# Kernel optimization log

Hardware: AMD Instinct MI355X
Metric: run time of the kernel (lower is better)

The kernel has to match this reference:

```python
import jax, jax.numpy as jnp
import numpy as np

CHUNK = 2048  # row tile size; keeps the [CHUNK, M] tile ~268 MB


def setup_inputs() -> dict:
    key = jax.random.key(0)
    k1, k2, k3 = jax.random.split(key, 3)
    N, M, D = 32768, 32768, 32
    ls = jax.random.uniform(k1, (1,), dtype=jnp.float32, minval=0.1, maxval=1.0)
    x = jax.random.normal(k2, (N, D), dtype=jnp.float32)
    y = jax.random.normal(k3, (M, D), dtype=jnp.float32)
    return {"ls": ls, "x": x, "y": y}


def reference(ls, x, y):
    # out[i] = sum_j exp(-ls * ||x_i - y_j||^2), computed in row tiles
    # (never materializes the full N x M matrix, like KeOps Genred).
    N, D = x.shape
    y_sq = jnp.sum(y * y, axis=1)  # [M]

    def row_chunk(xc):
        # xc: [CHUNK, D]
        x_sq = jnp.sum(xc * xc, axis=1)  # [CHUNK]
        sq = x_sq[:, None] + y_sq[None, :] - 2.0 * (xc @ y.T)  # [CHUNK, M]
        return jnp.sum(jnp.exp(-ls[0] * sq), axis=1)  # [CHUNK]

    x_tiles = x.reshape(N // CHUNK, CHUNK, D)
    out = jax.lax.map(row_chunk, x_tiles)  # [N//CHUNK, CHUNK]
    return out.reshape(N, 1)
```

## Files before the change

### kernel.cpp

```cpp
#include <hip/hip_runtime.h>
#include <math.h>

#define DIM 32
#define BLK 256
#define JSPLIT 16
#define ITPB 8
#define RI   2
#define GTT  16

typedef _Float16 half8 __attribute__((ext_vector_type(8)));
typedef float    f32x4 __attribute__((ext_vector_type(4)));
typedef float    f32x2 __attribute__((ext_vector_type(2)));

struct hl16 { half8 h; half8 l; };


__global__ __launch_bounds__(BLK) void rbf_prep(
    const float* __restrict__ lsp, const float* __restrict__ x,
    const float* __restrict__ y, int n, int m,
    double* __restrict__ acc, double* __restrict__ scale,
    float* __restrict__ bf, hl16* __restrict__ xhl, hl16* __restrict__ yhl)
{
    int i = blockIdx.x * BLK + threadIdx.x;
    const double c2 = -(double)lsp[0] * 1.4426950408889634074;
    const float mf = (float)(-2.0 * c2);
    if (i < n) {
        const float* xp = x + (size_t)i * DIM;
        double xs = 0.0;
        #pragma unroll
        for (int d = 0; d < DIM; ++d) { double v = (double)xp[d]; xs = fma(v, v, xs); }
        acc[i] = 0.0;
        scale[i] = exp2(c2 * xs);
        const int it = i >> 4, r15 = i & 15;
        #pragma unroll
        for (int q = 0; q < 4; ++q) {
            half8 hh, hl;
            #pragma unroll
            for (int d = 0; d < 8; ++d) {
                float v = xp[q * 8 + d] * mf;
                _Float16 h = (_Float16)v;
                hh[d] = h;
                hl[d] = (_Float16)((v - (float)h) * 4096.0f);
            }
            xhl[it * 64 + q * 16 + r15].h = hh;
            xhl[it * 64 + q * 16 + r15].l = hl;
        }
    }
    if (i < m) {
        const float* yp = y + (size_t)i * DIM;
        double ys = 0.0;
        #pragma unroll
        for (int d = 0; d < DIM; ++d) { double v = (double)yp[d]; ys = fma(v, v, ys); }
        bf[i] = (float)(c2 * ys);
        const int it = i >> 4, r15 = i & 15;
        #pragma unroll
        for (int q = 0; q < 4; ++q) {
            half8 hh, hl;
            #pragma unroll
            for (int d = 0; d < 8; ++d) {
                float v = yp[q * 8 + d];
                _Float16 h = (_Float16)v;
                hh[d] = h;
                hl[d] = (_Float16)((v - (float)h) * 4096.0f);
            }
            yhl[it * 64 + q * 16 + r15].h = hh;
            yhl[it * 64 + q * 16 + r15].l = hl;
        }
    }
}

__global__ __launch_bounds__(BLK, 4) void rbf_main(
    const hl16* __restrict__ xhl, const hl16* __restrict__ yhl,
    const float* __restrict__ bf, double* __restrict__ acc, int chunk_j)
{
    const int lane = threadIdx.x & 63;
    const int wave = threadIdx.x >> 6;
    const int itbase = blockIdx.x * ITPB + wave * RI;
    const int c15 = lane & 15;

    half8 ah[RI], al[RI];
    #pragma unroll
    for (int r = 0; r < RI; ++r) {
        ah[r] = xhl[(itbase + r) * 64 + lane].h;
        al[r] = xhl[(itbase + r) * 64 + lane].l;
    }

    const int jt0 = (blockIdx.y * chunk_j) >> 4;
    const int njt = chunk_j >> 4;

    const f32x4 zq = {0.0f, 0.0f, 0.0f, 0.0f};
    const float k12 = 0x1p-12f;

    double accd[RI][4];
    #pragma unroll
    for (int r = 0; r < RI; ++r)
        #pragma unroll
        for (int e = 0; e < 4; ++e) accd[r][e] = 0.0;

    half8 bh = yhl[(size_t)jt0 * 64 + lane].h;
    half8 bl = yhl[(size_t)jt0 * 64 + lane].l;
    float bfv = bf[jt0 * 16 + c15];

    for (int g = 0; g < njt / GTT; ++g) {
        f32x2 accf[RI][2];
        #pragma unroll
        for (int r = 0; r < RI; ++r) {
            accf[r][0] = (f32x2){0.0f, 0.0f};
            accf[r][1] = (f32x2){0.0f, 0.0f};
        }

        #pragma unroll
        for (int tt = 0; tt < GTT; ++tt) {
            const int jt = jt0 + g * GTT + tt;
            int jn = jt + 1; if (jn >= jt0 + njt) jn = jt0;
            const hl16* __restrict__ yt = yhl + (size_t)jn * 64;
            half8 bh_n = yt[lane].h;
            half8 bl_n = yt[lane].l;
            float bf_n = (bf + jn * 16)[c15];

            const f32x4 cbf = {bfv, bfv, bfv, bfv};
            #pragma unroll
            for (int r = 0; r < RI; ++r) {
                f32x4 cm = __builtin_amdgcn_mfma_f32_16x16x32_f16(ah[r], bh, cbf, 0, 0, 0);
                f32x4 cl = __builtin_amdgcn_mfma_f32_16x16x32_f16(ah[r], bl, zq, 0, 0, 0);
                cl = __builtin_amdgcn_mfma_f32_16x16x32_f16(al[r], bh, cl, 0, 0, 0);
                f32x2 f0 = {cm[0], cm[1]}, f1 = {cm[2], cm[3]};
                f32x2 l0 = {cl[0], cl[1]}, l1 = {cl[2], cl[3]};
                f0 = l0 * k12 + f0;
                f1 = l1 * k12 + f1;
                f32x2 e0 = {__builtin_amdgcn_exp2f(f0.x), __builtin_amdgcn_exp2f(f0.y)};
                f32x2 e1 = {__builtin_amdgcn_exp2f(f1.x), __builtin_amdgcn_exp2f(f1.y)};
                accf[r][0] += e0;
                accf[r][1] += e1;
            }
            bh = bh_n; bl = bl_n; bfv = bf_n;
        }
        #pragma unroll
        for (int r = 0; r < RI; ++r) {
            accd[r][0] += (double)accf[r][0].x;
            accd[r][1] += (double)accf[r][0].y;
            accd[r][2] += (double)accf[r][1].x;
            accd[r][3] += (double)accf[r][1].y;
        }
    }

    #pragma unroll
    for (int r = 0; r < RI; ++r) {
        #pragma unroll
        for (int e = 0; e < 4; ++e) {
            double v = accd[r][e];
            v += __shfl_xor(v, 1, 64);
            v += __shfl_xor(v, 2, 64);
            v += __shfl_xor(v, 4, 64);
            v += __shfl_xor(v, 8, 64);
            if (c15 == 0) {
                int row = (itbase + r) * 16 + (lane >> 4) * 4 + e;
                atomicAdd(&acc[row], v);
            }
        }
    }
}

__global__ __launch_bounds__(BLK) void rbf_finish(
    const double* __restrict__ acc, const double* __restrict__ scale,
    float* __restrict__ out, int n)
{
    int i = blockIdx.x * BLK + threadIdx.x;
    if (i < n) out[i] = (float)(acc[i] * scale[i]);
}

extern "C" void kernel_launch(void* const* d_in, const int* in_sizes, int n_in,
                              void* d_out, int out_size, void* d_ws, size_t ws_size,
                              hipStream_t stream)
{
    const float* ls = (const float*)d_in[0];
    const float* x  = (const float*)d_in[1];
    const float* y  = (const float*)d_in[2];
    const int n = in_sizes[1] / DIM;
    const int m = in_sizes[2] / DIM;
    float* out = (float*)d_out;

    char* ws = (char*)d_ws;
    double* acc   = (double*)ws;
    double* scale = acc + n;
    float*  bf    = (float*)(scale + n);
    hl16*   xhl   = (hl16*)(bf + m);
    hl16*   yhl   = xhl + (size_t)(n / 16) * 64;

    const int nm = (n > m) ? n : m;
    rbf_prep<<<(nm + BLK - 1) / BLK, BLK, 0, stream>>>(
        ls, x, y, n, m, acc, scale, bf, xhl, yhl);

    const int chunk = m / JSPLIT;
    dim3 grid(n / (16 * ITPB), JSPLIT);
    rbf_main<<<grid, BLK, 0, stream>>>(xhl, yhl, bf, acc, chunk);

    rbf_finish<<<(n + BLK - 1) / BLK, BLK, 0, stream>>>(acc, scale, out, n);
}
```

Before: 322.3 us.

## Fuse finish into main kernel, deepen y-tile prefetch, fold bias into low MFMA

Removes the separate finish kernel. Each row-block group now counts completed j-splits with an atomic counter, and the last block scales and writes the outputs itself. The y-tile loads move to a 4-slot ring buffer that prefetches two tiles ahead instead of one. The pre-scaled bias now seeds the low-part MFMA accumulator instead of the main one, and the occupancy hint drops from 4 to 3 blocks per CU. In exchange the code adds fences and atomics at block end and more live registers, and the prefetch reads two tiles past each chunk, which is why the workspace is reordered so y data comes before x data.

```diff
diff --git a/kernel.cpp b/kernel.cpp
--- a/kernel.cpp
+++ b/kernel.cpp
@@ -4,8 +4,8 @@
 #define DIM 32
 #define BLK 256
 #define JSPLIT 16
-#define ITPB 8
 #define RI   2
+#define ITPB (4*RI)
 #define GTT  16
 
 typedef _Float16 half8 __attribute__((ext_vector_type(8)));
@@ -19,11 +19,13 @@
     const float* __restrict__ lsp, const float* __restrict__ x,
     const float* __restrict__ y, int n, int m,
     double* __restrict__ acc, double* __restrict__ scale,
-    float* __restrict__ bf, hl16* __restrict__ xhl, hl16* __restrict__ yhl)
+    float* __restrict__ bfq, hl16* __restrict__ xhl, hl16* __restrict__ yhl,
+    int* __restrict__ cnt)
 {
     int i = blockIdx.x * BLK + threadIdx.x;
     const double c2 = -(double)lsp[0] * 1.4426950408889634074;
     const float mf = (float)(-2.0 * c2);
+    if (i < n / (16 * ITPB)) cnt[i] = 0;
     if (i < n) {
         const float* xp = x + (size_t)i * DIM;
         double xs = 0.0;
@@ -51,7 +53,7 @@
         double ys = 0.0;
         #pragma unroll
         for (int d = 0; d < DIM; ++d) { double v = (double)yp[d]; ys = fma(v, v, ys); }
-        bf[i] = (float)(c2 * ys);
+        bfq[i] = (float)(c2 * ys) * 4096.0f;
         const int it = i >> 4, r15 = i & 15;
         #pragma unroll
         for (int q = 0; q < 4; ++q) {
@@ -69,9 +71,11 @@
     }
 }
 
-__global__ __launch_bounds__(BLK, 4) void rbf_main(
+__global__ __launch_bounds__(BLK, 3) void rbf_main(
     const hl16* __restrict__ xhl, const hl16* __restrict__ yhl,
-    const float* __restrict__ bf, double* __restrict__ acc, int chunk_j)
+    const float* __restrict__ bfq, const double* __restrict__ scale,
+    double* __restrict__ acc, int* __restrict__ cnt,
+    float* __restrict__ out, int chunk_j)
 {
     const int lane = threadIdx.x & 63;
     const int wave = threadIdx.x >> 6;
@@ -97,9 +101,13 @@
         #pragma unroll
         for (int e = 0; e < 4; ++e) accd[r][e] = 0.0;
 
-    half8 bh = yhl[(size_t)jt0 * 64 + lane].h;
-    half8 bl = yhl[(size_t)jt0 * 64 + lane].l;
-    float bfv = bf[jt0 * 16 + c15];
+    const hl16*  __restrict__ ybase = yhl + (size_t)jt0 * 64;
+    const float* __restrict__ bbase = bfq + jt0 * 16;
+
+    half8 bh[4], bl[4];
+    float bq[4];
+    bh[0] = ybase[lane].h;      bl[0] = ybase[lane].l;      bq[0] = bbase[c15];
+    bh[1] = ybase[64 + lane].h; bl[1] = ybase[64 + lane].l; bq[1] = bbase[16 + c15];
 
     for (int g = 0; g < njt / GTT; ++g) {
         f32x2 accf[RI][2];
@@ -111,29 +119,28 @@
 
         #pragma unroll
         for (int tt = 0; tt < GTT; ++tt) {
-            const int jt = jt0 + g * GTT + tt;
-            int jn = jt + 1; if (jn >= jt0 + njt) jn = jt0;
-            const hl16* __restrict__ yt = yhl + (size_t)jn * 64;
-            half8 bh_n = yt[lane].h;
-            half8 bl_n = yt[lane].l;
-            float bf_n = (bf + jn * 16)[c15];
-
-            const f32x4 cbf = {bfv, bfv, bfv, bfv};
+            const int sc = tt & 3;
+            const int sp = (tt + 2) & 3;
+            const int pidx = g * GTT + tt + 2;
+            bh[sp] = ybase[(size_t)pidx * 64 + lane].h;
+            bl[sp] = ybase[(size_t)pidx * 64 + lane].l;
+            bq[sp] = bbase[pidx * 16 + c15];
+
+            const f32x4 bqq = {bq[sc], bq[sc], bq[sc], bq[sc]};
             #pragma unroll
             for (int r = 0; r < RI; ++r) {
-                f32x4 cm = __builtin_amdgcn_mfma_f32_16x16x32_f16(ah[r], bh, cbf, 0, 0, 0);
-                f32x4 cl = __builtin_amdgcn_mfma_f32_16x16x32_f16(ah[r], bl, zq, 0, 0, 0);
-                cl = __builtin_amdgcn_mfma_f32_16x16x32_f16(al[r], bh, cl, 0, 0, 0);
-                f32x2 f0 = {cm[0], cm[1]}, f1 = {cm[2], cm[3]};
-                f32x2 l0 = {cl[0], cl[1]}, l1 = {cl[2], cl[3]};
-                f0 = l0 * k12 + f0;
-                f1 = l1 * k12 + f1;
-                f32x2 e0 = {__builtin_amdgcn_exp2f(f0.x), __builtin_amdgcn_exp2f(f0.y)};
-                f32x2 e1 = {__builtin_amdgcn_exp2f(f1.x), __builtin_amdgcn_exp2f(f1.y)};
-                accf[r][0] += e0;
-                accf[r][1] += e1;
-            }
-            bh = bh_n; bl = bl_n; bfv = bf_n;
+                f32x4 cm = __builtin_amdgcn_mfma_f32_16x16x32_f16(ah[r], bh[sc], zq, 0, 0, 0);
+                f32x4 cl = __builtin_amdgcn_mfma_f32_16x16x32_f16(al[r], bh[sc], bqq, 0, 0, 0);
+                cl = __builtin_amdgcn_mfma_f32_16x16x32_f16(ah[r], bl[sc], cl, 0, 0, 0);
+                f32x2 cm01 = {cm[0], cm[1]}, cm23 = {cm[2], cm[3]};
+                f32x2 cl01 = {cl[0], cl[1]}, cl23 = {cl[2], cl[3]};
+                f32x2 f01 = cl01 * k12 + cm01;
+                f32x2 f23 = cl23 * k12 + cm23;
+                f32x2 e01 = {__builtin_amdgcn_exp2f(f01.x), __builtin_amdgcn_exp2f(f01.y)};
+                f32x2 e23 = {__builtin_amdgcn_exp2f(f23.x), __builtin_amdgcn_exp2f(f23.y)};
+                accf[r][0] += e01;
+                accf[r][1] += e23;
+            }
         }
         #pragma unroll
         for (int r = 0; r < RI; ++r) {
@@ -159,14 +166,24 @@
             }
         }
     }
-}
-
-__global__ __launch_bounds__(BLK) void rbf_finish(
-    const double* __restrict__ acc, const double* __restrict__ scale,
-    float* __restrict__ out, int n)
-{
-    int i = blockIdx.x * BLK + threadIdx.x;
-    if (i < n) out[i] = (float)(acc[i] * scale[i]);
+
+    __shared__ int lastflag;
+    __syncthreads();
+    if (threadIdx.x == 0) {
+        __threadfence();
+        int old = atomicAdd(&cnt[blockIdx.x], 1);
+        lastflag = (old == JSPLIT - 1);
+    }
+    __syncthreads();
+    if (lastflag) {
+        __threadfence();
+        const int rbase = blockIdx.x * (16 * ITPB);
+        if (threadIdx.x < 16 * ITPB) {
+            const int row = rbase + threadIdx.x;
+            double a = atomicAdd(&acc[row], 0.0);
+            out[row] = (float)(a * scale[row]);
+        }
+    }
 }
 
 extern "C" void kernel_launch(void* const* d_in, const int* in_sizes, int n_in,
@@ -183,17 +200,16 @@
     char* ws = (char*)d_ws;
     double* acc   = (double*)ws;
     double* scale = acc + n;
-    float*  bf    = (float*)(scale + n);
-    hl16*   xhl   = (hl16*)(bf + m);
-    hl16*   yhl   = xhl + (size_t)(n / 16) * 64;
+    float*  bfq   = (float*)(scale + n);
+    hl16*   yhl   = (hl16*)(bfq + m);
+    hl16*   xhl   = yhl + (size_t)(m / 16) * 64;
+    int*    cnt   = (int*)(xhl + (size_t)(n / 16) * 64);
 
     const int nm = (n > m) ? n : m;
     rbf_prep<<<(nm + BLK - 1) / BLK, BLK, 0, stream>>>(
-        ls, x, y, n, m, acc, scale, bf, xhl, yhl);
+        ls, x, y, n, m, acc, scale, bfq, xhl, yhl, cnt);
 
     const int chunk = m / JSPLIT;
     dim3 grid(n / (16 * ITPB), JSPLIT);
-    rbf_main<<<grid, BLK, 0, stream>>>(xhl, yhl, bf, acc, chunk);
-
-    rbf_finish<<<(n + BLK - 1) / BLK, BLK, 0, stream>>>(acc, scale, out, n);
+    rbf_main<<<grid, BLK, 0, stream>>>(xhl, yhl, bfq, scale, acc, cnt, out, chunk);
 }
```

New measurement: 373.8 us. +16.0%, slower.
